# Kernel tuning notes

Hardware: AMD Instinct MI355X
Metric: run time of the kernel (lower is better)

The kernel has to match this reference:

```python
import jax, jax.numpy as jnp
import numpy as np

NHEAD = 16
NUM_GROUPS = 4
EXPERTS_PER_GROUP = 2
LN_EPS = 1e-5


def _layernorm(x, g, b):
    mu = jnp.mean(x, axis=-1, keepdims=True)
    var = jnp.mean(jnp.square(x - mu), axis=-1, keepdims=True)
    return (x - mu) * jax.lax.rsqrt(var + LN_EPS) * g + b


def _mha(x, wi, bi, wo, bo):
    # torch nn.MultiheadAttention (batch_first): qkv = x @ in_proj_w.T + in_proj_b
    B, S, D = x.shape
    hd = D // NHEAD
    qkv = x @ wi.T + bi                      # [B,S,3D]
    q, k, v = jnp.split(qkv, 3, axis=-1)
    def heads(t):
        return t.reshape(B, S, NHEAD, hd).transpose(0, 2, 1, 3)  # [B,H,S,hd]
    q, k, v = heads(q), heads(k), heads(v)
    scores = jnp.einsum('bhqd,bhkd->bhqk', q, k) / jnp.sqrt(jnp.asarray(hd, x.dtype))
    attn = jax.nn.softmax(scores, axis=-1)
    o = jnp.einsum('bhqk,bhkd->bhqd', attn, v)
    o = o.transpose(0, 2, 1, 3).reshape(B, S, D)
    return o @ wo.T + bo


def _hier_moe(x, w_group, b_group, w_expert, b_expert, w1, b1, w2, b2):
    # Two-level top-1 routing: group gate -> expert gate within chosen group.
    B, S, D = x.shape
    xt = x.reshape(B * S, D)                 # [T,D]
    T = xt.shape[0]
    E = NUM_GROUPS * EXPERTS_PER_GROUP

    gp = jax.nn.softmax(xt @ w_group + b_group, axis=-1)          # [T,G]
    g_idx = jnp.argmax(gp, axis=-1)                                # [T]
    g_prob = jnp.max(gp, axis=-1)                                  # [T]

    elog = jnp.einsum('td,gde->tge', xt, w_expert) + b_expert      # [T,G,Epg]
    ep = jax.nn.softmax(elog, axis=-1)
    ep_sel = jnp.take_along_axis(ep, g_idx[:, None, None], axis=1)[:, 0, :]  # [T,Epg]
    e_idx_local = jnp.argmax(ep_sel, axis=-1)                      # [T]
    e_prob = jnp.max(ep_sel, axis=-1)                              # [T]

    flat_e = g_idx * EXPERTS_PER_GROUP + e_idx_local               # [T]
    combine = jax.nn.one_hot(flat_e, E, dtype=xt.dtype) * (g_prob * e_prob)[:, None]  # [T,E]

    # Dense dispatch (reference): run every expert on all tokens, combine with one-hot weights.
    h = jax.nn.relu(jnp.einsum('td,edf->etf', xt, w1) + b1[:, None, :])   # [E,T,Fff]
    y = jnp.einsum('etf,efd->etd', h, w2) + b2[:, None, :]                # [E,T,D]
    out = jnp.einsum('te,etd->td', combine, y)                            # [T,D]
    return out.reshape(B, S, D)


def setup_inputs() -> dict:
    key = jax.random.key(0)
    ks = jax.random.split(key, 8)
    B, S, D, F = 2, 1024, 1024, 2048
    G, Epg = NUM_GROUPS, EXPERTS_PER_GROUP
    E = G * Epg
    sc = lambda fan: 1.0 / np.sqrt(fan)
    return {
        'x': jax.random.normal(ks[0], (B, S, D), jnp.float32),
        'in_proj_w': jax.random.normal(ks[1], (3 * D, D), jnp.float32) * sc(D),
        'in_proj_b': jnp.zeros((3 * D,), jnp.float32),
        'out_proj_w': jax.random.normal(ks[2], (D, D), jnp.float32) * sc(D),
        'out_proj_b': jnp.zeros((D,), jnp.float32),
        'ln1_g': jnp.ones((D,), jnp.float32),
        'ln1_b': jnp.zeros((D,), jnp.float32),
        'ln2_g': jnp.ones((D,), jnp.float32),
        'ln2_b': jnp.zeros((D,), jnp.float32),
        'w_group': jax.random.normal(ks[3], (D, G), jnp.float32) * sc(D),
        'b_group': jnp.zeros((G,), jnp.float32),
        'w_expert': jax.random.normal(ks[4], (G, D, Epg), jnp.float32) * sc(D),
        'b_expert': jnp.zeros((G, Epg), jnp.float32),
        'w1': jax.random.normal(ks[5], (E, D, F), jnp.float32) * sc(D),
        'b1': jnp.zeros((E, F), jnp.float32),
        'w2': jax.random.normal(ks[6], (E, F, D), jnp.float32) * sc(F),
        'b2': jnp.zeros((E, D), jnp.float32),
    }


def reference(x, in_proj_w, in_proj_b, out_proj_w, out_proj_b,
              ln1_g, ln1_b, ln2_g, ln2_b,
              w_group, b_group, w_expert, b_expert, w1, b1, w2, b2):
    # Dropout p=0.1 is identity in eval mode.
    attn_out = _mha(x, in_proj_w, in_proj_b, out_proj_w, out_proj_b)
    x = _layernorm(x + attn_out, ln1_g, ln1_b)
    moe_out = _hier_moe(x, w_group, b_group, w_expert, b_expert, w1, b1, w2, b2)
    x = _layernorm(x + moe_out, ln2_g, ln2_b)
    return x
```

## Files before the change

### kernel.cpp

```cpp
#include <hip/hip_runtime.h>
#include <hip/hip_bf16.h>

#define TT 2048
#define DD 1024
#define FF 2048
#define SS 1024
#define NHD 16
#define HDD 64
#define NG 4
#define EPG 2
#define NE 8

#define QSC 0.18033688011112042f

typedef __attribute__((ext_vector_type(8))) short bf16x8;
typedef __attribute__((ext_vector_type(4))) float f32x4;
typedef __attribute__((ext_vector_type(4))) unsigned short ush4;

__device__ __forceinline__ unsigned short f2bf(float x) {
    unsigned int u = __float_as_uint(x);
    u = (u + 0x7fffu + ((u >> 16) & 1u)) >> 16;
    return (unsigned short)u;
}
__device__ __forceinline__ float bf2f(unsigned short h) {
    return __uint_as_float((unsigned int)h << 16);
}

__device__ __forceinline__ float wave_sum(float s) {
#pragma unroll
    for (int off = 32; off > 0; off >>= 1) s += __shfl_xor(s, off);
    return s;
}

__device__ __forceinline__ void gl16(const void* g, void* l) {
    auto gp = reinterpret_cast<const unsigned int __attribute__((address_space(1)))*>(
        (unsigned long long)g);
    auto lp = reinterpret_cast<unsigned int __attribute__((address_space(3)))*>(
        (unsigned int)(unsigned long long)l);
    __builtin_amdgcn_global_load_lds(gp, lp, 16, 0, 0);
}

__global__ __launch_bounds__(256) void split_bf16_kernel(
    const float* __restrict__ in, unsigned short* __restrict__ hi,
    unsigned short* __restrict__ lo, int n4)
{
    const int i = blockIdx.x * 256 + threadIdx.x;
    if (i >= n4) return;
    const float4 v = ((const float4*)in)[i];
    float vv[4] = {v.x, v.y, v.z, v.w};
    ush4 h, l;
#pragma unroll
    for (int j = 0; j < 4; ++j) {
        const unsigned short hb = f2bf(vv[j]);
        ((unsigned short*)&h)[j] = hb;
        ((unsigned short*)&l)[j] = f2bf(vv[j] - bf2f(hb));
    }
    ((ush4*)hi)[i] = h;
    ((ush4*)lo)[i] = l;
}

__global__ __launch_bounds__(256, 3) void gemm_split_kernel(
    const unsigned short* __restrict__ Ah, const unsigned short* __restrict__ Al,
    const unsigned short* __restrict__ Bh, const unsigned short* __restrict__ Bl,
    const float* __restrict__ bias, const float* __restrict__ resid,
    float* __restrict__ C, unsigned short* __restrict__ Chi,
    unsigned short* __restrict__ Clo, int qscale_n, int M, int N, int K)
{
    __shared__ unsigned short sAh[128 * 64];
    __shared__ unsigned short sAl[128 * 64];
    __shared__ unsigned short sBh[64 * 64];
    __shared__ unsigned short sBl[64 * 64];
    const int tid = threadIdx.x;
    const int lane = tid & 63, wid = tid >> 6;
    const int l15 = lane & 15, lg = lane >> 4;
    const int n0 = blockIdx.x << 6, m0 = blockIdx.y << 7;
    const int kper = K / gridDim.z;
    const int kbeg = blockIdx.z * kper, kend = kbeg + kper;
    float* __restrict__ Cz = C ? (C + (size_t)blockIdx.z * M * N) : C;

    f32x4 acc[2][4];
#pragma unroll
    for (int mi = 0; mi < 2; ++mi)
#pragma unroll
        for (int ni = 0; ni < 4; ++ni) acc[mi][ni] = (f32x4){0.f, 0.f, 0.f, 0.f};

    for (int k0 = kbeg; k0 < kend; k0 += 64) {
#pragma unroll
        for (int r = 0; r < 4; ++r) {
            const int s = (r << 8) + tid;
            const int row = s >> 3;
            const int cs = (s & 7) ^ (row & 7);
            const int lb = (s & ~63) << 3;
            const size_t ga = (size_t)(m0 + row) * K + k0 + (cs << 3);
            gl16(Ah + ga, &sAh[lb]);
            gl16(Al + ga, &sAl[lb]);
        }
#pragma unroll
        for (int r = 0; r < 2; ++r) {
            const int s = (r << 8) + tid;
            const int row = s >> 3;
            const int cs = (s & 7) ^ (row & 7);
            const int lb = (s & ~63) << 3;
            const size_t gb = (size_t)(n0 + row) * K + k0 + (cs << 3);
            gl16(Bh + gb, &sBh[lb]);
            gl16(Bl + gb, &sBl[lb]);
        }
        __syncthreads();
#pragma unroll
        for (int ks = 0; ks < 2; ++ks) {
            bf16x8 ah[2], al[2], bh[4], bl[4];
            const int ac = (ks << 2) + lg;
#pragma unroll
            for (int i = 0; i < 2; ++i) {
                const int ar = (wid << 5) + (i << 4) + l15;
                const int pa = ((ar << 3) | (ac ^ (ar & 7))) << 3;
                ah[i] = *(const bf16x8*)&sAh[pa];
                al[i] = *(const bf16x8*)&sAl[pa];
            }
#pragma unroll
            for (int i = 0; i < 4; ++i) {
                const int br = (i << 4) + l15;
                const int pb = ((br << 3) | (ac ^ (br & 7))) << 3;
                bh[i] = *(const bf16x8*)&sBh[pb];
                bl[i] = *(const bf16x8*)&sBl[pb];
            }
#pragma unroll
            for (int mi = 0; mi < 2; ++mi)
#pragma unroll
                for (int ni = 0; ni < 4; ++ni) {
                    acc[mi][ni] = __builtin_amdgcn_mfma_f32_16x16x32_bf16(ah[mi], bh[ni], acc[mi][ni], 0, 0, 0);
                    acc[mi][ni] = __builtin_amdgcn_mfma_f32_16x16x32_bf16(ah[mi], bl[ni], acc[mi][ni], 0, 0, 0);
                    acc[mi][ni] = __builtin_amdgcn_mfma_f32_16x16x32_bf16(al[mi], bh[ni], acc[mi][ni], 0, 0, 0);
                }
        }
        __syncthreads();
    }
#pragma unroll
    for (int mi = 0; mi < 2; ++mi)
#pragma unroll
        for (int ni = 0; ni < 4; ++ni)
#pragma unroll
            for (int r2 = 0; r2 < 4; ++r2) {
                const int m = m0 + (wid << 5) + (mi << 4) + (lg << 2) + r2;
                const int n = n0 + (ni << 4) + l15;
                float v = acc[mi][ni][r2];
                if (bias) v += bias[n];
                if (resid) v += resid[(size_t)m * N + n];
                const size_t idx = (size_t)m * N + n;
                if (Chi) {
                    if (n < qscale_n) v *= QSC;
                    const unsigned short hb = f2bf(v);
                    Chi[idx] = hb;
                    Clo[idx] = f2bf(v - bf2f(hb));
                } else {
                    Cz[idx] = v;
                }
            }
}

__global__ __launch_bounds__(256) void vtrans_kernel(
    const unsigned short* __restrict__ src, unsigned short* __restrict__ dst)
{
    __shared__ unsigned short tile[64][65];
    const int bh = blockIdx.y, b = bh >> 4, h = bh & 15;
    const int s0 = blockIdx.x << 6;
    const int tid = threadIdx.x;
#pragma unroll
    for (int r = 0; r < 2; ++r) {
        const int sl = tid + (r << 8);
        const int rr = sl >> 3, c8 = (sl & 7) << 3;
        const bf16x8 v = *(const bf16x8*)(src + (size_t)(b * SS + s0 + rr) * 3072 + 2048 + h * HDD + c8);
#pragma unroll
        for (int j = 0; j < 8; ++j) tile[rr][c8 + j] = ((const unsigned short*)&v)[j];
    }
    __syncthreads();
#pragma unroll
    for (int r = 0; r < 2; ++r) {
        const int sl = tid + (r << 8);
        const int d = sl >> 3, s8 = (sl & 7) << 3;
        bf16x8 o;
#pragma unroll
        for (int j = 0; j < 8; ++j) ((unsigned short*)&o)[j] = tile[s8 + j][d];
        *(bf16x8*)(dst + (size_t)(bh * HDD + d) * SS + s0 + s8) = o;
    }
}

__global__ __launch_bounds__(256, 4) void attn_mfma_kernel(
    const unsigned short* __restrict__ qh, const unsigned short* __restrict__ ql,
    const unsigned short* __restrict__ vth, const unsigned short* __restrict__ vtl,
    float* __restrict__ opart, float* __restrict__ mpart, float* __restrict__ lpart)
{
    __shared__ unsigned short sKh[4096], sKl[4096];
    __shared__ unsigned short sVh[4096], sVl[4096];
    const int bh = blockIdx.y, b = bh >> 4, h = bh & 15;
    const int q0 = blockIdx.x << 6;
    const int z = blockIdx.z;
    const int tid = threadIdx.x, lane = tid & 63, w = tid >> 6;
    const int l15 = lane & 15, lg = lane >> 4;

#pragma unroll
    for (int r = 0; r < 2; ++r) {
        const int s = (r << 8) + tid;
        const int row = s >> 3;
        const int cs = (s & 7) ^ (row & 7);
        const int lb = (s & ~63) << 3;
        const size_t gq = (size_t)(b * SS + q0 + row) * 3072 + h * HDD + (cs << 3);
        gl16(qh + gq, &sKh[lb]);
        gl16(ql + gq, &sKl[lb]);
    }
    __syncthreads();
    bf16x8 qah[2], qal[2];
#pragma unroll
    for (int ks = 0; ks < 2; ++ks) {
        const int ar = (w << 4) + l15;
        const int ac = (ks << 2) + lg;
        const int pa = ((ar << 3) | (ac ^ (ar & 7))) << 3;
// ... 135 lines not shown
    const int b = t >> 10, q = t & 1023;
    const int d0 = tid << 2;
    const int bh = (b << 4) + (d0 >> 6);
    const int mi = bh * SS + q;
    const float m0 = mpart[mi], m1 = mpart[32 * SS + mi];
    const float l0 = lpart[mi], l1 = lpart[32 * SS + mi];
    const float m = fmaxf(m0, m1);
    const float e0 = exp2f(m0 - m), e1 = exp2f(m1 - m);
    const float inv = 1.0f / (l0 * e0 + l1 * e1);
    const float4 a = *(const float4*)(opart + (size_t)t * DD + d0);
    const float4 c = *(const float4*)(opart + (size_t)(TT + t) * DD + d0);
    const float vv[4] = { (a.x * e0 + c.x * e1) * inv, (a.y * e0 + c.y * e1) * inv,
                          (a.z * e0 + c.z * e1) * inv, (a.w * e0 + c.w * e1) * inv };
    ush4 hh, ll;
#pragma unroll
    for (int j = 0; j < 4; ++j) {
        const unsigned short hb = f2bf(vv[j]);
        hh[j] = hb;
        ll[j] = f2bf(vv[j] - bf2f(hb));
    }
    *(ush4*)(ohi + (size_t)t * DD + d0) = hh;
    *(ush4*)(olo + (size_t)t * DD + d0) = ll;
}

__global__ __launch_bounds__(256) void ln_kernel(
    const float* __restrict__ in, const float* __restrict__ gamma,
    const float* __restrict__ beta, float* __restrict__ outf)
{
    const int t = blockIdx.x;
    const int tid = threadIdx.x;
    __shared__ float red[8];
    const float4 v = ((const float4*)(in + (size_t)t * DD))[tid];
    float s = v.x + v.y + v.z + v.w;
    s = wave_sum(s);
    const int wid = tid >> 6, lane = tid & 63;
    if (lane == 0) red[wid] = s;
    __syncthreads();
    const float mu = (red[0] + red[1] + red[2] + red[3]) * (1.0f / DD);
    const float d0 = v.x - mu, d1 = v.y - mu, d2 = v.z - mu, d3 = v.w - mu;
    float q = d0 * d0 + d1 * d1 + d2 * d2 + d3 * d3;
    q = wave_sum(q);
    if (lane == 0) red[4 + wid] = q;
    __syncthreads();
    const float var = (red[4] + red[5] + red[6] + red[7]) * (1.0f / DD);
    const float rstd = 1.0f / sqrtf(var + 1e-5f);
    const float4 g4 = ((const float4*)gamma)[tid];
    const float4 b4 = ((const float4*)beta)[tid];
    float4 ov = { d0 * rstd * g4.x + b4.x, d1 * rstd * g4.y + b4.y,
                  d2 * rstd * g4.z + b4.z, d3 * rstd * g4.w + b4.w };
    ((float4*)(outf + (size_t)t * DD))[tid] = ov;
}

__global__ __launch_bounds__(256) void ln_route_kernel(
    const float* __restrict__ x, const float* __restrict__ p0,
    const float* __restrict__ p1, const float* __restrict__ bo,
    const float* __restrict__ gamma, const float* __restrict__ beta,
    float* __restrict__ outf, unsigned short* __restrict__ outb,
    const float* __restrict__ wg, const float* __restrict__ bg,
    const float* __restrict__ we, const float* __restrict__ be,
    int* __restrict__ eid, float* __restrict__ gate, int* __restrict__ counts)
{
    const int t = blockIdx.x;
    const int tid = threadIdx.x;
    __shared__ float red[8];
    __shared__ float red2[4][12];
    const float4 xv = ((const float4*)(x + (size_t)t * DD))[tid];
    const float4 a4 = ((const float4*)(p0 + (size_t)t * DD))[tid];
    const float4 c4v = ((const float4*)(p1 + (size_t)t * DD))[tid];
    const float4 bo4 = ((const float4*)bo)[tid];
    const float4 v = { xv.x + a4.x + c4v.x + bo4.x, xv.y + a4.y + c4v.y + bo4.y,
                       xv.z + a4.z + c4v.z + bo4.z, xv.w + a4.w + c4v.w + bo4.w };
    float s = v.x + v.y + v.z + v.w;
    s = wave_sum(s);
    const int wid = tid >> 6, lane = tid & 63;
    if (lane == 0) red[wid] = s;
    __syncthreads();
    const float mu = (red[0] + red[1] + red[2] + red[3]) * (1.0f / DD);
    const float d0 = v.x - mu, d1 = v.y - mu, d2 = v.z - mu, d3 = v.w - mu;
    float q = d0 * d0 + d1 * d1 + d2 * d2 + d3 * d3;
    q = wave_sum(q);
    if (lane == 0) red[4 + wid] = q;
    __syncthreads();
    const float var = (red[4] + red[5] + red[6] + red[7]) * (1.0f / DD);
    const float rstd = 1.0f / sqrtf(var + 1e-5f);
    const float4 g4 = ((const float4*)gamma)[tid];
    const float4 b4 = ((const float4*)beta)[tid];
    const float o0 = d0 * rstd * g4.x + b4.x;
    const float o1 = d1 * rstd * g4.y + b4.y;
    const float o2 = d2 * rstd * g4.z + b4.z;
    const float o3 = d3 * rstd * g4.w + b4.w;
    float4 ov = {o0, o1, o2, o3};
    ((float4*)(outf + (size_t)t * DD))[tid] = ov;
    ush4 wv = { f2bf(o0), f2bf(o1), f2bf(o2), f2bf(o3) };
    *(ush4*)(outb + (size_t)t * DD + (tid << 2)) = wv;

    float pz[12];
#pragma unroll
    for (int k = 0; k < 12; ++k) pz[k] = 0.f;
    const float xo[4] = {o0, o1, o2, o3};
#pragma unroll
    for (int j = 0; j < 4; ++j) {
        const int c = (tid << 2) + j;
        const float xvv = xo[j];
        const float4 wgv = *(const float4*)(wg + c * NG);
        pz[0] = fmaf(xvv, wgv.x, pz[0]);
        pz[1] = fmaf(xvv, wgv.y, pz[1]);
        pz[2] = fmaf(xvv, wgv.z, pz[2]);
        pz[3] = fmaf(xvv, wgv.w, pz[3]);
#pragma unroll
        for (int g = 0; g < NG; ++g) {
            const float2 wev = *(const float2*)(we + ((size_t)g * DD + c) * EPG);
            pz[4 + 2 * g]     = fmaf(xvv, wev.x, pz[4 + 2 * g]);
            pz[4 + 2 * g + 1] = fmaf(xvv, wev.y, pz[4 + 2 * g + 1]);
        }
    }
#pragma unroll
    for (int k = 0; k < 12; ++k) pz[k] = wave_sum(pz[k]);
    if (lane == 0) {
#pragma unroll
        for (int k = 0; k < 12; ++k) red2[wid][k] = pz[k];
    }
    __syncthreads();
    if (tid == 0) {
        float zs[12];
#pragma unroll
        for (int k = 0; k < 12; ++k)
            zs[k] = red2[0][k] + red2[1][k] + red2[2][k] + red2[3][k];
        float z[NG];
#pragma unroll
        for (int g = 0; g < NG; ++g) z[g] = zs[g] + bg[g];
        int gi = 0; float zb = z[0];
#pragma unroll
        for (int g = 1; g < NG; ++g) if (z[g] > zb) { zb = z[g]; gi = g; }
        float se = 0.f;
#pragma unroll
        for (int g = 0; g < NG; ++g) se += __expf(z[g] - zb);
        const float gprob = 1.0f / se;
        float e0 = 0.f, e1 = 0.f;
#pragma unroll
        for (int g = 0; g < NG; ++g) {
            if (g == gi) {
                e0 = zs[4 + 2 * g] + be[g * EPG + 0];
                e1 = zs[4 + 2 * g + 1] + be[g * EPG + 1];
            }
        }
        const int ei = (e1 > e0) ? 1 : 0;
        const float ehi = ei ? e1 : e0, elo = ei ? e0 : e1;
        const float eprob = 1.0f / (1.0f + __expf(elo - ehi));
        eid[t] = gi * EPG + ei;
        gate[t] = gprob * eprob;
        atomicAdd(&counts[gi * EPG + ei], 1);
    }
}

__global__ void zero_counts_kernel(int* __restrict__ counts) {
    if (threadIdx.x < NE) counts[threadIdx.x] = 0;
}

__global__ void offsets_kernel(const int* __restrict__ counts, int* __restrict__ offs,
                               int* __restrict__ cursor) {
    if (threadIdx.x == 0) {
        int run = 0;
        for (int e = 0; e < NE; ++e) { offs[e] = run; cursor[e] = run; run += counts[e]; }
        offs[NE] = run;
    }
}

__global__ __launch_bounds__(256) void scatter_kernel(const int* __restrict__ eid,
                                                      int* __restrict__ cursor,
                                                      int* __restrict__ perm) {
    const int t = blockIdx.x * 256 + threadIdx.x;
    const int slot = atomicAdd(&cursor[eid[t]], 1);
    perm[slot] = t;
}

__global__ __launch_bounds__(256) void transpose_bf16_kernel(
    const float* __restrict__ in, unsigned short* __restrict__ out, int R, int C)
{
    __shared__ float tile[32][33];
    const int c0 = blockIdx.x << 5, r0 = blockIdx.y << 5;
    const size_t bo = (size_t)blockIdx.z * R * C;
    const int tc = threadIdx.x & 31, tr8 = threadIdx.x >> 5;
#pragma unroll
    for (int p = 0; p < 4; ++p) {
        const int rr = tr8 + (p << 3);
        tile[rr][tc] = in[bo + (size_t)(r0 + rr) * C + c0 + tc];
    }
    __syncthreads();
#pragma unroll
    for (int p = 0; p < 4; ++p) {
        const int rr = tr8 + (p << 3);
        out[bo + (size_t)(c0 + rr) * R + r0 + tc] = f2bf(tile[tc][rr]);
    }
}

__global__ __launch_bounds__(256, 4) void moe_gemm1_kernel(
    const unsigned short* __restrict__ x1b, const unsigned short* __restrict__ w1t,
    const float* __restrict__ b1, const int* __restrict__ offs,
    const int* __restrict__ perm, unsigned short* __restrict__ hbuf)
{
    const int e = blockIdx.y >> 5, mt = blockIdx.y & 31;
    const int row0 = offs[e] + (mt << 6);
    const int rend = offs[e + 1];
    if (row0 >= rend) return;
    const int valid = min(rend - row0, 64);
    const int n0 = blockIdx.x << 6;
    __shared__ unsigned short sA[2][64 * 64];
    __shared__ unsigned short sB[2][64 * 64];
    const int tid = threadIdx.x;
    const int lane = tid & 63, w = tid >> 6;
    const int l15 = lane & 15, lg = lane >> 4;

    size_t abase[2], bbase[2];
    int lbs[2];
#pragma unroll
    for (int r = 0; r < 2; ++r) {
        const int s = (r << 8) + tid;
        const int row = s >> 3;
        const int cs = (s & 7) ^ (row & 7);
        lbs[r] = (s & ~63) << 3;
        const int tk = perm[min(row0 + row, rend - 1)];
        abase[r] = (size_t)tk * DD + (cs << 3);
        bbase[r] = ((size_t)e * FF + n0 + row) * DD + (cs << 3);
    }

    f32x4 acc[4];
#pragma unroll
    for (int nt = 0; nt < 4; ++nt) acc[nt] = (f32x4){0.f, 0.f, 0.f, 0.f};

#pragma unroll
    for (int r = 0; r < 2; ++r) {
        gl16(x1b + abase[r], &sA[0][lbs[r]]);
        gl16(w1t + bbase[r], &sB[0][lbs[r]]);
    }
    __syncthreads();
    int cur = 0;
    for (int k0 = 0; k0 < DD; k0 += 64) {
        const int nxt = k0 + 64;
        if (nxt < DD) {
#pragma unroll
            for (int r = 0; r < 2; ++r) {
                gl16(x1b + abase[r] + nxt, &sA[cur ^ 1][lbs[r]]);
                gl16(w1t + bbase[r] + nxt, &sB[cur ^ 1][lbs[r]]);
            }
        }
#pragma unroll
        for (int ks = 0; ks < 2; ++ks) {
            const int ac = (ks << 2) + lg;
            const int ar = (w << 4) + l15;
            const int pa = ((ar << 3) | (ac ^ (ar & 7))) << 3;
            const bf16x8 a = *(const bf16x8*)&sA[cur][pa];
#pragma unroll
            for (int nt = 0; nt < 4; ++nt) {
                const int br = (nt << 4) + l15;
                const int pb = ((br << 3) | (ac ^ (br & 7))) << 3;
                acc[nt] = __builtin_amdgcn_mfma_f32_16x16x32_bf16(
                    a, *(const bf16x8*)&sB[cur][pb], acc[nt], 0, 0, 0);
            }
        }
        __syncthreads();
        cur ^= 1;
    }

    const float* bias = b1 + e * FF + n0;
    const int mbase = (w << 4) + (lg << 2);
#pragma unroll
    for (int nt = 0; nt < 4; ++nt) {
        const int n = (nt << 4) + l15;
#pragma unroll
        for (int r2 = 0; r2 < 4; ++r2) {
            const int m = mbase + r2;
            if (m < valid) {
                float v = fmaxf(acc[nt][r2] + bias[n], 0.f);
                hbuf[(size_t)(row0 + m) * FF + n0 + n] = f2bf(v);
            }
        }
    }
}

__global__ __launch_bounds__(256, 4) void moe_gemm2_kernel(
    const unsigned short* __restrict__ hbuf, const unsigned short* __restrict__ w2t,
    const int* __restrict__ offs, float* __restrict__ p0, float* __restrict__ p1)
{
    const int e = blockIdx.y >> 5, mt = blockIdx.y & 31;
    const int row0 = offs[e] + (mt << 6);
    const int rend = offs[e + 1];
    if (row0 >= rend) return;
    const int valid = min(rend - row0, 64);
    const int n0 = blockIdx.x << 6;
    const int z = blockIdx.z;
    float* __restrict__ pbuf = z ? p1 : p0;
    __shared__ unsigned short sA[2][64 * 64];
    __shared__ unsigned short sB[2][64 * 64];
    const int tid = threadIdx.x;
    const int lane = tid & 63, w = tid >> 6;
    const int l15 = lane & 15, lg = lane >> 4;

    size_t abase[2], bbase[2];
    int lbs[2];
#pragma unroll
    for (int r = 0; r < 2; ++r) {
        const int s = (r << 8) + tid;
        const int row = s >> 3;
        const int cs = (s & 7) ^ (row & 7);
        lbs[r] = (s & ~63) << 3;
        abase[r] = (size_t)(row0 + row) * FF + (cs << 3);
        bbase[r] = ((size_t)e * DD + n0 + row) * FF + (cs << 3);
    }

    f32x4 acc[4];
#pragma unroll
    for (int nt = 0; nt < 4; ++nt) acc[nt] = (f32x4){0.f, 0.f, 0.f, 0.f};

    const int kbeg = z << 10, kend = kbeg + 1024;
#pragma unroll
    for (int r = 0; r < 2; ++r) {
        gl16(hbuf + abase[r] + kbeg, &sA[0][lbs[r]]);
        gl16(w2t + bbase[r] + kbeg, &sB[0][lbs[r]]);
    }
    __syncthreads();
    int cur = 0;
    for (int k0 = kbeg; k0 < kend; k0 += 64) {
        const int nxt = k0 + 64;
        if (nxt < kend) {
#pragma unroll
            for (int r = 0; r < 2; ++r) {
                gl16(hbuf + abase[r] + nxt, &sA[cur ^ 1][lbs[r]]);
                gl16(w2t + bbase[r] + nxt, &sB[cur ^ 1][lbs[r]]);
            }
        }
#pragma unroll
        for (int ks = 0; ks < 2; ++ks) {
            const int ac = (ks << 2) + lg;
            const int ar = (w << 4) + l15;
            const int pa = ((ar << 3) | (ac ^ (ar & 7))) << 3;
            const bf16x8 a = *(const bf16x8*)&sA[cur][pa];
#pragma unroll
            for (int nt = 0; nt < 4; ++nt) {
                const int br = (nt << 4) + l15;
                const int pb = ((br << 3) | (ac ^ (br & 7))) << 3;
                acc[nt] = __builtin_amdgcn_mfma_f32_16x16x32_bf16(
                    a, *(const bf16x8*)&sB[cur][pb], acc[nt], 0, 0, 0);
            }
        }
        __syncthreads();
        cur ^= 1;
    }

    const int mbase = (w << 4) + (lg << 2);
#pragma unroll
    for (int nt = 0; nt < 4; ++nt) {
        const int n = (nt << 4) + l15;
#pragma unroll
        for (int r2 = 0; r2 < 4; ++r2) {
            const int m = mbase + r2;
            if (m < valid) pbuf[(size_t)(row0 + m) * DD + n0 + n] = acc[nt][r2];
        }
    }
}

__global__ __launch_bounds__(256) void moe2_combine_kernel(
    const float* __restrict__ p0, const float* __restrict__ p1,
    const int* __restrict__ offs, const int* __restrict__ perm,
    const float* __restrict__ gate, const float* __restrict__ b2,
    const float* __restrict__ x1, float* __restrict__ res2)
{
    const int s = blockIdx.x;
    const int tid = threadIdx.x;
    int e = 0;
#pragma unroll
    for (int g = 1; g < NE; ++g) e += (s >= offs[g]) ? 1 : 0;
    const int tk = perm[s];
    const float gt = gate[tk];
    const int c0 = tid << 2;
    const float4 a  = *(const float4*)(p0 + (size_t)s * DD + c0);
    const float4 b  = *(const float4*)(p1 + (size_t)s * DD + c0);
    const float4 bb = *(const float4*)(b2 + (size_t)e * DD + c0);
    const float4 xx = *(const float4*)(x1 + (size_t)tk * DD + c0);
    float4 o = { xx.x + gt * (a.x + b.x + bb.x), xx.y + gt * (a.y + b.y + bb.y),
                 xx.z + gt * (a.z + b.z + bb.z), xx.w + gt * (a.w + b.w + bb.w) };
    *(float4*)(res2 + (size_t)tk * DD + c0) = o;
}

extern "C" void kernel_launch(void* const* d_in, const int* in_sizes, int n_in,
                              void* d_out, int out_size, void* d_ws, size_t ws_size,
                              hipStream_t stream)
{
    (void)in_sizes; (void)n_in; (void)out_size; (void)ws_size;
    const float* x   = (const float*)d_in[0];
    const float* wi  = (const float*)d_in[1];
    const float* bi  = (const float*)d_in[2];
    const float* wo  = (const float*)d_in[3];
    const float* bo  = (const float*)d_in[4];
    const float* g1  = (const float*)d_in[5];
    const float* be1 = (const float*)d_in[6];
    const float* g2  = (const float*)d_in[7];
    const float* be2 = (const float*)d_in[8];
    const float* wgr = (const float*)d_in[9];
    const float* bgr = (const float*)d_in[10];
    const float* wex = (const float*)d_in[11];
    const float* bex = (const float*)d_in[12];
    const float* w1  = (const float*)d_in[13];
    const float* b1  = (const float*)d_in[14];
    const float* w2  = (const float*)d_in[15];
    const float* b2  = (const float*)d_in[16];
    float* out = (float*)d_out;

    char* ws = (char*)d_ws;
    unsigned short* qkvh  = (unsigned short*)(ws + 0);
    unsigned short* qkvl  = (unsigned short*)(ws + 12582912);
    unsigned short* hbuf  = (unsigned short*)(ws + 0);
    float* res2           = (float*)(ws + 8388608);
    unsigned short* vth   = (unsigned short*)(ws + 25165824);
    unsigned short* vtl   = (unsigned short*)(ws + 29360128);
    float* x1             = (float*)(ws + 41943040);
    unsigned short* x1b   = (unsigned short*)(ws + 50331648);
    unsigned short* w1t   = (unsigned short*)(ws + 54525952);
    unsigned short* w2t   = (unsigned short*)(ws + 88080384);
    char* misc = ws + 121634816;
    int*   eid    = (int*)(misc);
    float* gate   = (float*)(misc + 8192);
    int*   perm   = (int*)(misc + 16384);
    int*   counts = (int*)(misc + 24576);
    int*   offs   = (int*)(misc + 24640);
    int*   cursor = (int*)(misc + 24704);

    unsigned short* xs_hi = (unsigned short*)(ws + 33554432);
    unsigned short* xs_lo = (unsigned short*)(ws + 33554432 + 4194304);
    unsigned short* wi_hi = (unsigned short*)(ws + 54525952);
    unsigned short* wi_lo = (unsigned short*)(ws + 54525952 + 6291456);
    unsigned short* o_hi  = (unsigned short*)(ws + 41943040);
    unsigned short* o_lo  = (unsigned short*)(ws + 41943040 + 4194304);
    unsigned short* wo_hi = (unsigned short*)(ws + 88080384);
    unsigned short* wo_lo = (unsigned short*)(ws + 88080384 + 2097152);

    float* opart = (float*)(ws + 54525952);
    float* mpart = (float*)(ws + 54525952 + 16777216);
    float* lpart = (float*)(ws + 54525952 + 17039360);

    float* oproj = (float*)(ws + 0);

    float* mp0 = (float*)(ws + 16777216);
    float* mp1 = (float*)(ws + 25165824);

    zero_counts_kernel<<<dim3(1), dim3(64), 0, stream>>>(counts);

    split_bf16_kernel<<<dim3((TT * DD / 4 + 255) / 256), dim3(256), 0, stream>>>(x, xs_hi, xs_lo, TT * DD / 4);
    split_bf16_kernel<<<dim3((3 * DD * DD / 4 + 255) / 256), dim3(256), 0, stream>>>(wi, wi_hi, wi_lo, 3 * DD * DD / 4);
    gemm_split_kernel<<<dim3(3 * DD / 64, TT / 128, 1), dim3(256), 0, stream>>>(
        xs_hi, xs_lo, wi_hi, wi_lo, bi, (const float*)nullptr,
        (float*)nullptr, qkvh, qkvl, DD, TT, 3 * DD, DD);

    vtrans_kernel<<<dim3(SS / 64, 2 * NHD), dim3(256), 0, stream>>>(qkvh, vth);
    vtrans_kernel<<<dim3(SS / 64, 2 * NHD), dim3(256), 0, stream>>>(qkvl, vtl);

    attn_mfma_kernel<<<dim3(SS / 64, 2 * NHD, 2), dim3(256), 0, stream>>>(
        qkvh, qkvl, vth, vtl, opart, mpart, lpart);
    attn_combine_kernel<<<dim3(TT), dim3(256), 0, stream>>>(opart, mpart, lpart, o_hi, o_lo);

    split_bf16_kernel<<<dim3((DD * DD / 4 + 255) / 256), dim3(256), 0, stream>>>(wo, wo_hi, wo_lo, DD * DD / 4);
    gemm_split_kernel<<<dim3(DD / 64, TT / 128, 2), dim3(256), 0, stream>>>(
        o_hi, o_lo, wo_hi, wo_lo, (const float*)nullptr, (const float*)nullptr,
        oproj, (unsigned short*)nullptr, (unsigned short*)nullptr, 0, TT, DD, DD);

    ln_route_kernel<<<dim3(TT), dim3(256), 0, stream>>>(
        x, oproj, oproj + (size_t)TT * DD, bo, g1, be1, x1, x1b,
        wgr, bgr, wex, bex, eid, gate, counts);
    offsets_kernel<<<dim3(1), dim3(64), 0, stream>>>(counts, offs, cursor);
    scatter_kernel<<<dim3(TT / 256), dim3(256), 0, stream>>>(eid, cursor, perm);

    transpose_bf16_kernel<<<dim3(FF / 32, DD / 32, NE), dim3(256), 0, stream>>>(w1, w1t, DD, FF);
    transpose_bf16_kernel<<<dim3(DD / 32, FF / 32, NE), dim3(256), 0, stream>>>(w2, w2t, FF, DD);

    moe_gemm1_kernel<<<dim3(FF / 64, NE * 32), dim3(256), 0, stream>>>(x1b, w1t, b1, offs, perm, hbuf);
    moe_gemm2_kernel<<<dim3(DD / 64, NE * 32, 2), dim3(256), 0, stream>>>(hbuf, w2t, offs, mp0, mp1);
    moe2_combine_kernel<<<dim3(TT), dim3(256), 0, stream>>>(mp0, mp1, offs, perm, gate, b2, x1, res2);

    ln_kernel<<<dim3(TT), dim3(256), 0, stream>>>(res2, g2, be2, out);
}
```

Before: 273.7 us.

## Enlarge split-bf16 GEMM tiles, deepen out-proj split-K, merge small launches

The split-precision GEMM is templated on the N-tile width and uses a 2x2 wave layout with 128xNC block tiles (96 columns for the QKV projection, 128 for the output projection). This raises MFMA work per shared-memory load and improves operand reuse, at the cost of more registers and occupancy lowered to 2 blocks per CU. The output projection now uses 4-way split-K, and ln_route sums the four partials. The two V-transpose launches are merged into one grid with a z dimension, and the offsets and scatter kernels are fused into one single-block kernel that uses shared-memory atomics, which cuts launch overhead but serialises the scatter onto one block.

```diff
diff --git a/kernel.cpp b/kernel.cpp
--- a/kernel.cpp
+++ b/kernel.cpp
@@ -59,30 +59,33 @@
     ((ush4*)lo)[i] = l;
 }
 
-__global__ __launch_bounds__(256, 3) void gemm_split_kernel(
+template <int NI>
+__global__ __launch_bounds__(256, 2) void gemm_split_kernel(
     const unsigned short* __restrict__ Ah, const unsigned short* __restrict__ Al,
     const unsigned short* __restrict__ Bh, const unsigned short* __restrict__ Bl,
     const float* __restrict__ bias, const float* __restrict__ resid,
     float* __restrict__ C, unsigned short* __restrict__ Chi,
     unsigned short* __restrict__ Clo, int qscale_n, int M, int N, int K)
 {
+    constexpr int NC = NI * 32;
     __shared__ unsigned short sAh[128 * 64];
     __shared__ unsigned short sAl[128 * 64];
-    __shared__ unsigned short sBh[64 * 64];
-    __shared__ unsigned short sBl[64 * 64];
+    __shared__ unsigned short sBh[NC * 64];
+    __shared__ unsigned short sBl[NC * 64];
     const int tid = threadIdx.x;
     const int lane = tid & 63, wid = tid >> 6;
     const int l15 = lane & 15, lg = lane >> 4;
-    const int n0 = blockIdx.x << 6, m0 = blockIdx.y << 7;
+    const int wr = wid >> 1, wc = wid & 1;
+    const int n0 = blockIdx.x * NC, m0 = blockIdx.y << 7;
     const int kper = K / gridDim.z;
     const int kbeg = blockIdx.z * kper, kend = kbeg + kper;
     float* __restrict__ Cz = C ? (C + (size_t)blockIdx.z * M * N) : C;
 
-    f32x4 acc[2][4];
-#pragma unroll
-    for (int mi = 0; mi < 2; ++mi)
-#pragma unroll
-        for (int ni = 0; ni < 4; ++ni) acc[mi][ni] = (f32x4){0.f, 0.f, 0.f, 0.f};
+    f32x4 acc[4][NI];
+#pragma unroll
+    for (int mi = 0; mi < 4; ++mi)
+#pragma unroll
+        for (int ni = 0; ni < NI; ++ni) acc[mi][ni] = (f32x4){0.f, 0.f, 0.f, 0.f};
 
     for (int k0 = kbeg; k0 < kend; k0 += 64) {
 #pragma unroll
@@ -96,7 +99,7 @@
             gl16(Al + ga, &sAl[lb]);
         }
 #pragma unroll
-        for (int r = 0; r < 2; ++r) {
+        for (int r = 0; r < NC / 32; ++r) {
             const int s = (r << 8) + tid;
             const int row = s >> 3;
             const int cs = (s & 7) ^ (row & 7);
@@ -108,26 +111,26 @@
         __syncthreads();
 #pragma unroll
         for (int ks = 0; ks < 2; ++ks) {
-            bf16x8 ah[2], al[2], bh[4], bl[4];
             const int ac = (ks << 2) + lg;
-#pragma unroll
-            for (int i = 0; i < 2; ++i) {
-                const int ar = (wid << 5) + (i << 4) + l15;
+            bf16x8 ah[4], al[4], bh[NI], bl[NI];
+#pragma unroll
+            for (int mi = 0; mi < 4; ++mi) {
+                const int ar = (wr << 6) + (mi << 4) + l15;
                 const int pa = ((ar << 3) | (ac ^ (ar & 7))) << 3;
-                ah[i] = *(const bf16x8*)&sAh[pa];
-                al[i] = *(const bf16x8*)&sAl[pa];
-            }
-#pragma unroll
-            for (int i = 0; i < 4; ++i) {
-                const int br = (i << 4) + l15;
+                ah[mi] = *(const bf16x8*)&sAh[pa];
+                al[mi] = *(const bf16x8*)&sAl[pa];
+            }
+#pragma unroll
+            for (int ni = 0; ni < NI; ++ni) {
+                const int br = wc * (NI << 4) + (ni << 4) + l15;
                 const int pb = ((br << 3) | (ac ^ (br & 7))) << 3;
-                bh[i] = *(const bf16x8*)&sBh[pb];
-                bl[i] = *(const bf16x8*)&sBl[pb];
-            }
-#pragma unroll
-            for (int mi = 0; mi < 2; ++mi)
-#pragma unroll
-                for (int ni = 0; ni < 4; ++ni) {
+                bh[ni] = *(const bf16x8*)&sBh[pb];
+                bl[ni] = *(const bf16x8*)&sBl[pb];
+            }
+#pragma unroll
+            for (int mi = 0; mi < 4; ++mi)
+#pragma unroll
+                for (int ni = 0; ni < NI; ++ni) {
                     acc[mi][ni] = __builtin_amdgcn_mfma_f32_16x16x32_bf16(ah[mi], bh[ni], acc[mi][ni], 0, 0, 0);
                     acc[mi][ni] = __builtin_amdgcn_mfma_f32_16x16x32_bf16(ah[mi], bl[ni], acc[mi][ni], 0, 0, 0);
                     acc[mi][ni] = __builtin_amdgcn_mfma_f32_16x16x32_bf16(al[mi], bh[ni], acc[mi][ni], 0, 0, 0);
@@ -136,13 +139,13 @@
         __syncthreads();
     }
 #pragma unroll
-    for (int mi = 0; mi < 2; ++mi)
-#pragma unroll
-        for (int ni = 0; ni < 4; ++ni)
+    for (int mi = 0; mi < 4; ++mi)
+#pragma unroll
+        for (int ni = 0; ni < NI; ++ni)
 #pragma unroll
             for (int r2 = 0; r2 < 4; ++r2) {
-                const int m = m0 + (wid << 5) + (mi << 4) + (lg << 2) + r2;
-                const int n = n0 + (ni << 4) + l15;
+                const int m = m0 + (wr << 6) + (mi << 4) + (lg << 2) + r2;
+                const int n = n0 + wc * (NI << 4) + (ni << 4) + l15;
                 float v = acc[mi][ni][r2];
                 if (bias) v += bias[n];
                 if (resid) v += resid[(size_t)m * N + n];
@@ -159,9 +162,12 @@
 }
 
 __global__ __launch_bounds__(256) void vtrans_kernel(
-    const unsigned short* __restrict__ src, unsigned short* __restrict__ dst)
+    const unsigned short* __restrict__ srch, const unsigned short* __restrict__ srcl,
+    unsigned short* __restrict__ dsth, unsigned short* __restrict__ dstl)
 {
     __shared__ unsigned short tile[64][65];
+    const unsigned short* __restrict__ src = blockIdx.z ? srcl : srch;
+    unsigned short* __restrict__ dst = blockIdx.z ? dstl : dsth;
     const int bh = blockIdx.y, b = bh >> 4, h = bh & 15;
     const int s0 = blockIdx.x << 6;
     const int tid = threadIdx.x;
@@ -403,8 +409,8 @@
 }
 
 __global__ __launch_bounds__(256) void ln_route_kernel(
-    const float* __restrict__ x, const float* __restrict__ p0,
-    const float* __restrict__ p1, const float* __restrict__ bo,
+    const float* __restrict__ x, const float* __restrict__ op,
+    const float* __restrict__ bo,
     const float* __restrict__ gamma, const float* __restrict__ beta,
     float* __restrict__ outf, unsigned short* __restrict__ outb,
     const float* __restrict__ wg, const float* __restrict__ bg,
@@ -416,11 +422,13 @@
     __shared__ float red[8];
     __shared__ float red2[4][12];
     const float4 xv = ((const float4*)(x + (size_t)t * DD))[tid];
-    const float4 a4 = ((const float4*)(p0 + (size_t)t * DD))[tid];
-    const float4 c4v = ((const float4*)(p1 + (size_t)t * DD))[tid];
     const float4 bo4 = ((const float4*)bo)[tid];
-    const float4 v = { xv.x + a4.x + c4v.x + bo4.x, xv.y + a4.y + c4v.y + bo4.y,
-                       xv.z + a4.z + c4v.z + bo4.z, xv.w + a4.w + c4v.w + bo4.w };
+    float4 v = { xv.x + bo4.x, xv.y + bo4.y, xv.z + bo4.z, xv.w + bo4.w };
+#pragma unroll
+    for (int zz = 0; zz < 4; ++zz) {
+        const float4 p4 = ((const float4*)(op + (size_t)zz * TT * DD + (size_t)t * DD))[tid];
+        v.x += p4.x; v.y += p4.y; v.z += p4.z; v.w += p4.w;
+    }
     float s = v.x + v.y + v.z + v.w;
     s = wave_sum(s);
     const int wid = tid >> 6, lane = tid & 63;
@@ -508,21 +516,23 @@
     if (threadIdx.x < NE) counts[threadIdx.x] = 0;
 }
 
-__global__ void offsets_kernel(const int* __restrict__ counts, int* __restrict__ offs,
-                               int* __restrict__ cursor) {
+__global__ __launch_bounds__(256) void route_scatter_kernel(
+    const int* __restrict__ eid, const int* __restrict__ counts,
+    int* __restrict__ offs, int* __restrict__ perm)
+{
+    __shared__ int loff[NE + 1];
+    __shared__ int lcur[NE];
     if (threadIdx.x == 0) {
         int run = 0;
-        for (int e = 0; e < NE; ++e) { offs[e] = run; cursor[e] = run; run += counts[e]; }
-        offs[NE] = run;
-    }
-}
-
-__global__ __launch_bounds__(256) void scatter_kernel(const int* __restrict__ eid,
-                                                      int* __restrict__ cursor,
-                                                      int* __restrict__ perm) {
-    const int t = blockIdx.x * 256 + threadIdx.x;
-    const int slot = atomicAdd(&cursor[eid[t]], 1);
-    perm[slot] = t;
+        for (int e = 0; e < NE; ++e) { loff[e] = run; lcur[e] = run; run += counts[e]; }
+        loff[NE] = run;
+    }
+    __syncthreads();
+    for (int t = threadIdx.x; t < TT; t += 256) {
+        const int slot = atomicAdd(&lcur[eid[t]], 1);
+        perm[slot] = t;
+    }
+    if (threadIdx.x <= NE) offs[threadIdx.x] = loff[threadIdx.x];
 }
 
 __global__ __launch_bounds__(256) void transpose_bf16_kernel(
@@ -774,7 +784,6 @@
     int*   perm   = (int*)(misc + 16384);
     int*   counts = (int*)(misc + 24576);
     int*   offs   = (int*)(misc + 24640);
-    int*   cursor = (int*)(misc + 24704);
 
     unsigned short* xs_hi = (unsigned short*)(ws + 33554432);
     unsigned short* xs_lo = (unsigned short*)(ws + 33554432 + 4194304);
@@ -798,27 +807,24 @@
 
     split_bf16_kernel<<<dim3((TT * DD / 4 + 255) / 256), dim3(256), 0, stream>>>(x, xs_hi, xs_lo, TT * DD / 4);
     split_bf16_kernel<<<dim3((3 * DD * DD / 4 + 255) / 256), dim3(256), 0, stream>>>(wi, wi_hi, wi_lo, 3 * DD * DD / 4);
-    gemm_split_kernel<<<dim3(3 * DD / 64, TT / 128, 1), dim3(256), 0, stream>>>(
+    gemm_split_kernel<3><<<dim3(3 * DD / 96, TT / 128, 1), dim3(256), 0, stream>>>(
         xs_hi, xs_lo, wi_hi, wi_lo, bi, (const float*)nullptr,
         (float*)nullptr, qkvh, qkvl, DD, TT, 3 * DD, DD);
 
-    vtrans_kernel<<<dim3(SS / 64, 2 * NHD), dim3(256), 0, stream>>>(qkvh, vth);
-    vtrans_kernel<<<dim3(SS / 64, 2 * NHD), dim3(256), 0, stream>>>(qkvl, vtl);
+    vtrans_kernel<<<dim3(SS / 64, 2 * NHD, 2), dim3(256), 0, stream>>>(qkvh, qkvl, vth, vtl);
 
     attn_mfma_kernel<<<dim3(SS / 64, 2 * NHD, 2), dim3(256), 0, stream>>>(
         qkvh, qkvl, vth, vtl, opart, mpart, lpart);
     attn_combine_kernel<<<dim3(TT), dim3(256), 0, stream>>>(opart, mpart, lpart, o_hi, o_lo);
 
     split_bf16_kernel<<<dim3((DD * DD / 4 + 255) / 256), dim3(256), 0, stream>>>(wo, wo_hi, wo_lo, DD * DD / 4);
-    gemm_split_kernel<<<dim3(DD / 64, TT / 128, 2), dim3(256), 0, stream>>>(
+    gemm_split_kernel<4><<<dim3(DD / 128, TT / 128, 4), dim3(256), 0, stream>>>(
         o_hi, o_lo, wo_hi, wo_lo, (const float*)nullptr, (const float*)nullptr,
         oproj, (unsigned short*)nullptr, (unsigned short*)nullptr, 0, TT, DD, DD);
 
     ln_route_kernel<<<dim3(TT), dim3(256), 0, stream>>>(
-        x, oproj, oproj + (size_t)TT * DD, bo, g1, be1, x1, x1b,
-        wgr, bgr, wex, bex, eid, gate, counts);
-    offsets_kernel<<<dim3(1), dim3(64), 0, stream>>>(counts, offs, cursor);
-    scatter_kernel<<<dim3(TT / 256), dim3(256), 0, stream>>>(eid, cursor, perm);
+        x, oproj, bo, g1, be1, x1, x1b, wgr, bgr, wex, bex, eid, gate, counts);
+    route_scatter_kernel<<<dim3(1), dim3(256), 0, stream>>>(eid, counts, offs, perm);
 
     transpose_bf16_kernel<<<dim3(FF / 32, DD / 32, NE), dim3(256), 0, stream>>>(w1, w1t, DD, FF);
     transpose_bf16_kernel<<<dim3(DD / 32, FF / 32, NE), dim3(256), 0, stream>>>(w2, w2t, FF, DD);
```

After: 264.3 us. -3.4%, faster.

## Enlarge MoE GEMM tiles to 128 rows and merge routing and transpose launches

Applied to the files above, without the earlier changes.

Both MoE expert GEMMs move from 64x64 to 128x64 block tiles, with a 2x2 warp grid in which each warp computes a 64x32 sub-tile. This raises MFMA work per LDS fragment load and halves how often weight tiles are reloaded. The offsets and scatter kernels merge into one single-block kernel that uses shared-memory atomics, and the two V-transpose launches merge into one launch via blockIdx.z. The cost is more LDS and registers per block, so occupancy drops, and row padding is wasted on experts whose token counts are not multiples of 128.

```diff
diff --git a/kernel.cpp b/kernel.cpp
--- a/kernel.cpp
+++ b/kernel.cpp
@@ -159,9 +159,12 @@
 }
 
 __global__ __launch_bounds__(256) void vtrans_kernel(
-    const unsigned short* __restrict__ src, unsigned short* __restrict__ dst)
+    const unsigned short* __restrict__ srch, const unsigned short* __restrict__ srcl,
+    unsigned short* __restrict__ dsth, unsigned short* __restrict__ dstl)
 {
     __shared__ unsigned short tile[64][65];
+    const unsigned short* __restrict__ src = blockIdx.z ? srcl : srch;
+    unsigned short* __restrict__ dst = blockIdx.z ? dstl : dsth;
     const int bh = blockIdx.y, b = bh >> 4, h = bh & 15;
     const int s0 = blockIdx.x << 6;
     const int tid = threadIdx.x;
@@ -508,21 +511,23 @@
     if (threadIdx.x < NE) counts[threadIdx.x] = 0;
 }
 
-__global__ void offsets_kernel(const int* __restrict__ counts, int* __restrict__ offs,
-                               int* __restrict__ cursor) {
+__global__ __launch_bounds__(256) void route_scatter_kernel(
+    const int* __restrict__ eid, const int* __restrict__ counts,
+    int* __restrict__ offs, int* __restrict__ perm)
+{
+    __shared__ int loff[NE + 1];
+    __shared__ int lcur[NE];
     if (threadIdx.x == 0) {
         int run = 0;
-        for (int e = 0; e < NE; ++e) { offs[e] = run; cursor[e] = run; run += counts[e]; }
-        offs[NE] = run;
-    }
-}
-
-__global__ __launch_bounds__(256) void scatter_kernel(const int* __restrict__ eid,
-                                                      int* __restrict__ cursor,
-                                                      int* __restrict__ perm) {
-    const int t = blockIdx.x * 256 + threadIdx.x;
-    const int slot = atomicAdd(&cursor[eid[t]], 1);
-    perm[slot] = t;
+        for (int e = 0; e < NE; ++e) { loff[e] = run; lcur[e] = run; run += counts[e]; }
+        loff[NE] = run;
+    }
+    __syncthreads();
+    for (int t = threadIdx.x; t < TT; t += 256) {
+        const int slot = atomicAdd(&lcur[eid[t]], 1);
+        perm[slot] = t;
+    }
+    if (threadIdx.x <= NE) offs[threadIdx.x] = loff[threadIdx.x];
 }
 
 __global__ __launch_bounds__(256) void transpose_bf16_kernel(
@@ -545,169 +550,207 @@
     }
 }
 
-__global__ __launch_bounds__(256, 4) void moe_gemm1_kernel(
+__global__ __launch_bounds__(256, 3) void moe_gemm1_kernel(
     const unsigned short* __restrict__ x1b, const unsigned short* __restrict__ w1t,
     const float* __restrict__ b1, const int* __restrict__ offs,
     const int* __restrict__ perm, unsigned short* __restrict__ hbuf)
 {
-    const int e = blockIdx.y >> 5, mt = blockIdx.y & 31;
-    const int row0 = offs[e] + (mt << 6);
+    const int e = blockIdx.y >> 4, mt = blockIdx.y & 15;
+    const int row0 = offs[e] + (mt << 7);
     const int rend = offs[e + 1];
     if (row0 >= rend) return;
-    const int valid = min(rend - row0, 64);
+    const int valid = min(rend - row0, 128);
     const int n0 = blockIdx.x << 6;
-    __shared__ unsigned short sA[2][64 * 64];
+    __shared__ unsigned short sA[2][128 * 64];
     __shared__ unsigned short sB[2][64 * 64];
     const int tid = threadIdx.x;
-    const int lane = tid & 63, w = tid >> 6;
+    const int lane = tid & 63, wid = tid >> 6;
     const int l15 = lane & 15, lg = lane >> 4;
-
-    size_t abase[2], bbase[2];
-    int lbs[2];
+    const int wr = wid >> 1, wc = wid & 1;
+
+    size_t abase[4];
+    int albs[4];
+#pragma unroll
+    for (int r = 0; r < 4; ++r) {
+        const int s = (r << 8) + tid;
+        const int row = s >> 3;
+        const int cs = (s & 7) ^ (row & 7);
+        albs[r] = (s & ~63) << 3;
+        const int tk = perm[min(row0 + row, rend - 1)];
+        abase[r] = (size_t)tk * DD + (cs << 3);
+    }
+    size_t bbase[2];
+    int blbs[2];
 #pragma unroll
     for (int r = 0; r < 2; ++r) {
         const int s = (r << 8) + tid;
         const int row = s >> 3;
         const int cs = (s & 7) ^ (row & 7);
-        lbs[r] = (s & ~63) << 3;
-        const int tk = perm[min(row0 + row, rend - 1)];
-        abase[r] = (size_t)tk * DD + (cs << 3);
+        blbs[r] = (s & ~63) << 3;
         bbase[r] = ((size_t)e * FF + n0 + row) * DD + (cs << 3);
     }
 
-    f32x4 acc[4];
-#pragma unroll
-    for (int nt = 0; nt < 4; ++nt) acc[nt] = (f32x4){0.f, 0.f, 0.f, 0.f};
-
-#pragma unroll
-    for (int r = 0; r < 2; ++r) {
-        gl16(x1b + abase[r], &sA[0][lbs[r]]);
-        gl16(w1t + bbase[r], &sB[0][lbs[r]]);
-    }
+    f32x4 acc[4][2];
+#pragma unroll
+    for (int mi = 0; mi < 4; ++mi)
+#pragma unroll
+        for (int ni = 0; ni < 2; ++ni) acc[mi][ni] = (f32x4){0.f, 0.f, 0.f, 0.f};
+
+#pragma unroll
+    for (int r = 0; r < 4; ++r) gl16(x1b + abase[r], &sA[0][albs[r]]);
+#pragma unroll
+    for (int r = 0; r < 2; ++r) gl16(w1t + bbase[r], &sB[0][blbs[r]]);
     __syncthreads();
     int cur = 0;
     for (int k0 = 0; k0 < DD; k0 += 64) {
         const int nxt = k0 + 64;
         if (nxt < DD) {
 #pragma unroll
-            for (int r = 0; r < 2; ++r) {
-                gl16(x1b + abase[r] + nxt, &sA[cur ^ 1][lbs[r]]);
-                gl16(w1t + bbase[r] + nxt, &sB[cur ^ 1][lbs[r]]);
-            }
+            for (int r = 0; r < 4; ++r) gl16(x1b + abase[r] + nxt, &sA[cur ^ 1][albs[r]]);
+#pragma unroll
+            for (int r = 0; r < 2; ++r) gl16(w1t + bbase[r] + nxt, &sB[cur ^ 1][blbs[r]]);
         }
 #pragma unroll
         for (int ks = 0; ks < 2; ++ks) {
             const int ac = (ks << 2) + lg;
-            const int ar = (w << 4) + l15;
-            const int pa = ((ar << 3) | (ac ^ (ar & 7))) << 3;
-            const bf16x8 a = *(const bf16x8*)&sA[cur][pa];
-#pragma unroll
-            for (int nt = 0; nt < 4; ++nt) {
-                const int br = (nt << 4) + l15;
+            bf16x8 a[4], bb[2];
+#pragma unroll
+            for (int mi = 0; mi < 4; ++mi) {
+                const int ar = (wr << 6) + (mi << 4) + l15;
+                const int pa = ((ar << 3) | (ac ^ (ar & 7))) << 3;
+                a[mi] = *(const bf16x8*)&sA[cur][pa];
+            }
+#pragma unroll
+            for (int ni = 0; ni < 2; ++ni) {
+                const int br = (wc << 5) + (ni << 4) + l15;
                 const int pb = ((br << 3) | (ac ^ (br & 7))) << 3;
-                acc[nt] = __builtin_amdgcn_mfma_f32_16x16x32_bf16(
-                    a, *(const bf16x8*)&sB[cur][pb], acc[nt], 0, 0, 0);
-            }
+                bb[ni] = *(const bf16x8*)&sB[cur][pb];
+            }
+#pragma unroll
+            for (int mi = 0; mi < 4; ++mi)
+#pragma unroll
+                for (int ni = 0; ni < 2; ++ni)
+                    acc[mi][ni] = __builtin_amdgcn_mfma_f32_16x16x32_bf16(a[mi], bb[ni], acc[mi][ni], 0, 0, 0);
         }
         __syncthreads();
         cur ^= 1;
     }
 
     const float* bias = b1 + e * FF + n0;
-    const int mbase = (w << 4) + (lg << 2);
-#pragma unroll
-    for (int nt = 0; nt < 4; ++nt) {
-        const int n = (nt << 4) + l15;
-#pragma unroll
-        for (int r2 = 0; r2 < 4; ++r2) {
-            const int m = mbase + r2;
-            if (m < valid) {
-                float v = fmaxf(acc[nt][r2] + bias[n], 0.f);
-                hbuf[(size_t)(row0 + m) * FF + n0 + n] = f2bf(v);
-            }
-        }
-    }
-}
-
-__global__ __launch_bounds__(256, 4) void moe_gemm2_kernel(
+#pragma unroll
+    for (int mi = 0; mi < 4; ++mi)
+#pragma unroll
+        for (int ni = 0; ni < 2; ++ni) {
+            const int n = (wc << 5) + (ni << 4) + l15;
+#pragma unroll
+            for (int r2 = 0; r2 < 4; ++r2) {
+                const int m = (wr << 6) + (mi << 4) + (lg << 2) + r2;
+                if (m < valid) {
+                    float v = fmaxf(acc[mi][ni][r2] + bias[n], 0.f);
+                    hbuf[(size_t)(row0 + m) * FF + n0 + n] = f2bf(v);
+                }
+            }
+        }
+}
+
+__global__ __launch_bounds__(256, 3) void moe_gemm2_kernel(
     const unsigned short* __restrict__ hbuf, const unsigned short* __restrict__ w2t,
     const int* __restrict__ offs, float* __restrict__ p0, float* __restrict__ p1)
 {
-    const int e = blockIdx.y >> 5, mt = blockIdx.y & 31;
-    const int row0 = offs[e] + (mt << 6);
+    const int e = blockIdx.y >> 4, mt = blockIdx.y & 15;
+    const int row0 = offs[e] + (mt << 7);
     const int rend = offs[e + 1];
     if (row0 >= rend) return;
-    const int valid = min(rend - row0, 64);
+    const int valid = min(rend - row0, 128);
     const int n0 = blockIdx.x << 6;
     const int z = blockIdx.z;
     float* __restrict__ pbuf = z ? p1 : p0;
-    __shared__ unsigned short sA[2][64 * 64];
+    __shared__ unsigned short sA[2][128 * 64];
     __shared__ unsigned short sB[2][64 * 64];
     const int tid = threadIdx.x;
-    const int lane = tid & 63, w = tid >> 6;
+    const int lane = tid & 63, wid = tid >> 6;
     const int l15 = lane & 15, lg = lane >> 4;
-
-    size_t abase[2], bbase[2];
-    int lbs[2];
+    const int wr = wid >> 1, wc = wid & 1;
+
+    size_t abase[4];
+    int albs[4];
+#pragma unroll
+    for (int r = 0; r < 4; ++r) {
+        const int s = (r << 8) + tid;
+        const int row = s >> 3;
+        const int cs = (s & 7) ^ (row & 7);
+        albs[r] = (s & ~63) << 3;
+        abase[r] = (size_t)min(row0 + row, rend - 1) * FF + (cs << 3);
+    }
+    size_t bbase[2];
+    int blbs[2];
 #pragma unroll
     for (int r = 0; r < 2; ++r) {
         const int s = (r << 8) + tid;
         const int row = s >> 3;
         const int cs = (s & 7) ^ (row & 7);
-        lbs[r] = (s & ~63) << 3;
-        abase[r] = (size_t)(row0 + row) * FF + (cs << 3);
+        blbs[r] = (s & ~63) << 3;
         bbase[r] = ((size_t)e * DD + n0 + row) * FF + (cs << 3);
     }
 
-    f32x4 acc[4];
-#pragma unroll
-    for (int nt = 0; nt < 4; ++nt) acc[nt] = (f32x4){0.f, 0.f, 0.f, 0.f};
+    f32x4 acc[4][2];
+#pragma unroll
+    for (int mi = 0; mi < 4; ++mi)
+#pragma unroll
+        for (int ni = 0; ni < 2; ++ni) acc[mi][ni] = (f32x4){0.f, 0.f, 0.f, 0.f};
 
     const int kbeg = z << 10, kend = kbeg + 1024;
 #pragma unroll
-    for (int r = 0; r < 2; ++r) {
-        gl16(hbuf + abase[r] + kbeg, &sA[0][lbs[r]]);
-        gl16(w2t + bbase[r] + kbeg, &sB[0][lbs[r]]);
-    }
+    for (int r = 0; r < 4; ++r) gl16(hbuf + abase[r] + kbeg, &sA[0][albs[r]]);
+#pragma unroll
+    for (int r = 0; r < 2; ++r) gl16(w2t + bbase[r] + kbeg, &sB[0][blbs[r]]);
     __syncthreads();
     int cur = 0;
     for (int k0 = kbeg; k0 < kend; k0 += 64) {
         const int nxt = k0 + 64;
         if (nxt < kend) {
 #pragma unroll
-            for (int r = 0; r < 2; ++r) {
-                gl16(hbuf + abase[r] + nxt, &sA[cur ^ 1][lbs[r]]);
-                gl16(w2t + bbase[r] + nxt, &sB[cur ^ 1][lbs[r]]);
-            }
+            for (int r = 0; r < 4; ++r) gl16(hbuf + abase[r] + nxt, &sA[cur ^ 1][albs[r]]);
+#pragma unroll
+            for (int r = 0; r < 2; ++r) gl16(w2t + bbase[r] + nxt, &sB[cur ^ 1][blbs[r]]);
         }
 #pragma unroll
         for (int ks = 0; ks < 2; ++ks) {
             const int ac = (ks << 2) + lg;
-            const int ar = (w << 4) + l15;
-            const int pa = ((ar << 3) | (ac ^ (ar & 7))) << 3;
-            const bf16x8 a = *(const bf16x8*)&sA[cur][pa];
-#pragma unroll
-            for (int nt = 0; nt < 4; ++nt) {
-                const int br = (nt << 4) + l15;
+            bf16x8 a[4], bb[2];
+#pragma unroll
+            for (int mi = 0; mi < 4; ++mi) {
+                const int ar = (wr << 6) + (mi << 4) + l15;
+                const int pa = ((ar << 3) | (ac ^ (ar & 7))) << 3;
+                a[mi] = *(const bf16x8*)&sA[cur][pa];
+            }
+#pragma unroll
+            for (int ni = 0; ni < 2; ++ni) {
+                const int br = (wc << 5) + (ni << 4) + l15;
                 const int pb = ((br << 3) | (ac ^ (br & 7))) << 3;
-                acc[nt] = __builtin_amdgcn_mfma_f32_16x16x32_bf16(
-                    a, *(const bf16x8*)&sB[cur][pb], acc[nt], 0, 0, 0);
-            }
+                bb[ni] = *(const bf16x8*)&sB[cur][pb];
+            }
+#pragma unroll
+            for (int mi = 0; mi < 4; ++mi)
+#pragma unroll
+                for (int ni = 0; ni < 2; ++ni)
+                    acc[mi][ni] = __builtin_amdgcn_mfma_f32_16x16x32_bf16(a[mi], bb[ni], acc[mi][ni], 0, 0, 0);
         }
         __syncthreads();
         cur ^= 1;
     }
 
-    const int mbase = (w << 4) + (lg << 2);
-#pragma unroll
-    for (int nt = 0; nt < 4; ++nt) {
-        const int n = (nt << 4) + l15;
-#pragma unroll
-        for (int r2 = 0; r2 < 4; ++r2) {
-            const int m = mbase + r2;
-            if (m < valid) pbuf[(size_t)(row0 + m) * DD + n0 + n] = acc[nt][r2];
-        }
-    }
+#pragma unroll
+    for (int mi = 0; mi < 4; ++mi)
+#pragma unroll
+        for (int ni = 0; ni < 2; ++ni) {
+            const int n = (wc << 5) + (ni << 4) + l15;
+#pragma unroll
+            for (int r2 = 0; r2 < 4; ++r2) {
+                const int m = (wr << 6) + (mi << 4) + (lg << 2) + r2;
+                if (m < valid) pbuf[(size_t)(row0 + m) * DD + n0 + n] = acc[mi][ni][r2];
+            }
+        }
 }
 
 __global__ __launch_bounds__(256) void moe2_combine_kernel(
@@ -774,7 +817,6 @@
     int*   perm   = (int*)(misc + 16384);
     int*   counts = (int*)(misc + 24576);
     int*   offs   = (int*)(misc + 24640);
-    int*   cursor = (int*)(misc + 24704);
 
     unsigned short* xs_hi = (unsigned short*)(ws + 33554432);
     unsigned short* xs_lo = (unsigned short*)(ws + 33554432 + 4194304);
@@ -802,8 +844,7 @@
         xs_hi, xs_lo, wi_hi, wi_lo, bi, (const float*)nullptr,
         (float*)nullptr, qkvh, qkvl, DD, TT, 3 * DD, DD);
 
-    vtrans_kernel<<<dim3(SS / 64, 2 * NHD), dim3(256), 0, stream>>>(qkvh, vth);
-    vtrans_kernel<<<dim3(SS / 64, 2 * NHD), dim3(256), 0, stream>>>(qkvl, vtl);
+    vtrans_kernel<<<dim3(SS / 64, 2 * NHD, 2), dim3(256), 0, stream>>>(qkvh, qkvl, vth, vtl);
 
     attn_mfma_kernel<<<dim3(SS / 64, 2 * NHD, 2), dim3(256), 0, stream>>>(
         qkvh, qkvl, vth, vtl, opart, mpart, lpart);
@@ -817,14 +858,13 @@
     ln_route_kernel<<<dim3(TT), dim3(256), 0, stream>>>(
         x, oproj, oproj + (size_t)TT * DD, bo, g1, be1, x1, x1b,
         wgr, bgr, wex, bex, eid, gate, counts);
-    offsets_kernel<<<dim3(1), dim3(64), 0, stream>>>(counts, offs, cursor);
-    scatter_kernel<<<dim3(TT / 256), dim3(256), 0, stream>>>(eid, cursor, perm);
+    route_scatter_kernel<<<dim3(1), dim3(256), 0, stream>>>(eid, counts, offs, perm);
 
     transpose_bf16_kernel<<<dim3(FF / 32, DD / 32, NE), dim3(256), 0, stream>>>(w1, w1t, DD, FF);
     transpose_bf16_kernel<<<dim3(DD / 32, FF / 32, NE), dim3(256), 0, stream>>>(w2, w2t, FF, DD);
 
-    moe_gemm1_kernel<<<dim3(FF / 64, NE * 32), dim3(256), 0, stream>>>(x1b, w1t, b1, offs, perm, hbuf);
-    moe_gemm2_kernel<<<dim3(DD / 64, NE * 32, 2), dim3(256), 0, stream>>>(hbuf, w2t, offs, mp0, mp1);
+    moe_gemm1_kernel<<<dim3(FF / 64, NE * 16), dim3(256), 0, stream>>>(x1b, w1t, b1, offs, perm, hbuf);
+    moe_gemm2_kernel<<<dim3(DD / 64, NE * 16, 2), dim3(256), 0, stream>>>(hbuf, w2t, offs, mp0, mp1);
     moe2_combine_kernel<<<dim3(TT), dim3(256), 0, stream>>>(mp0, mp1, offs, perm, gate, b2, x1, res2);
 
     ln_kernel<<<dim3(TT), dim3(256), 0, stream>>>(res2, g2, be2, out);
```

Result: faster. 256.6 us (-6.2%).
